# Kernel optimization log

Measured on AMD Instinct MI355X. Metric: run time of the kernel, lower is better.

The kernel has to match this reference:

```python
import jax
import jax.numpy as jnp
import numpy as np
from jax import lax

B = 4096        # batch
DATA = 16       # data_dim (control channels)
HID = 64        # hidden_dim
VFW = 128       # vf_hidden_dim
LAB = 10        # label_dim
T = 201         # number of time points in ts (span [0,1])
DT0 = 0.01      # fixed step size -> 100 Heun steps over [0,1]
N_STEPS = 100


def _linear_init(key, out_f, in_f):
    kw, kb = jax.random.split(key)
    lim = 1.0 / np.sqrt(in_f)
    w = jax.random.uniform(kw, (out_f, in_f), minval=-lim, maxval=lim, dtype=jnp.float32)
    b = jax.random.uniform(kb, (out_f,), minval=-lim, maxval=lim, dtype=jnp.float32)
    return w, b


def setup_inputs() -> dict:
    key = jax.random.key(0)
    ks = jax.random.split(key, 8)
    ts = jnp.linspace(0.0, 1.0, T, dtype=jnp.float32)
    coeffs = jax.random.normal(ks[0], (T - 1, DATA, 4), dtype=jnp.float32) * 0.1
    x0 = jax.random.normal(ks[1], (B, DATA), dtype=jnp.float32)
    lin1_w, lin1_b = _linear_init(ks[2], HID, DATA)
    mlp_w0, mlp_b0 = _linear_init(ks[3], VFW, HID)
    mlp_w1, mlp_b1 = _linear_init(ks[4], VFW, VFW)
    mlp_w2, mlp_b2 = _linear_init(ks[5], HID * DATA, VFW)
    lin2_w, lin2_b = _linear_init(ks[6], LAB, HID)
    return dict(ts=ts, coeffs=coeffs, x0=x0,
                lin1_w=lin1_w, lin1_b=lin1_b,
                mlp_w0=mlp_w0, mlp_b0=mlp_b0,
                mlp_w1=mlp_w1, mlp_b1=mlp_b1,
                mlp_w2=mlp_w2, mlp_b2=mlp_b2,
                lin2_w=lin2_w, lin2_b=lin2_b)


def reference(ts, coeffs, x0, lin1_w, lin1_b, mlp_w0, mlp_b0, mlp_w1, mlp_b1,
              mlp_w2, mlp_b2, lin2_w, lin2_b):
    def control_deriv(t):
        # cubic spline segment lookup: coeffs[idx] is (DATA, 4)
        idx = jnp.clip(jnp.searchsorted(ts[1:], t), 0, T - 2)
        dt = t - ts[idx]
        c = coeffs[idx]
        return c[:, 0] + dt * (c[:, 1] + dt * (c[:, 2] + dt * c[:, 3]))  # (DATA,)

    def vector_field(t, y):
        # MLP: HID -> VFW -> VFW -> HID*DATA (relu, relu, tanh)
        h = jax.nn.relu(y @ mlp_w0.T + mlp_b0)
        h = jax.nn.relu(h @ mlp_w1.T + mlp_b1)
        h = jnp.tanh(h @ mlp_w2.T + mlp_b2)
        vf = h.reshape(-1, HID, DATA)            # (B, HID, DATA)
        cd = control_deriv(t)                    # (DATA,)
        return jnp.einsum('bhd,d->bh', vf, cd)   # dy/dt, (B, HID)

    y0 = x0 @ lin1_w.T + lin1_b                  # (B, HID)
    t0 = ts[0]
    t1 = ts[-1]
    dt = (t1 - t0) / N_STEPS                     # == DT0 for [0,1] span

    def step(carry, _):
        y, t = carry
        k1 = vector_field(t, y)
        k2 = vector_field(t + dt, y + dt * k1)
        y_next = y + 0.5 * dt * (k1 + k2)        # Heun (explicit trapezoidal)
        return (y_next, t + dt), None

    (y_final, _), _ = lax.scan(step, (y0, t0), None, length=N_STEPS)
    logits = y_final @ lin2_w.T + lin2_b
    return jax.nn.softmax(logits, axis=-1)       # (B, LAB)
```

## Files before the change

### kernel.cpp

```cpp
#include <hip/hip_runtime.h>

#define BTOT   4096
#define DATA   16
#define HID    64
#define VFW    128
#define LAB    10
#define TPTS   201
#define NSEG   200
#define NSTEPS 100
#define MT     16
#define NBLK   (BTOT / MT)
#define YS     68

typedef __attribute__((ext_vector_type(8))) short short8;
typedef __attribute__((ext_vector_type(4))) float f32x4;

#define LOG2E  1.4426950408889634f
#define K2L    (2.0f * LOG2E)

__device__ __forceinline__ short f2bf(float f) {
    unsigned u = __builtin_bit_cast(unsigned, f);
    u = (u + 0x7FFFu + ((u >> 16) & 1u)) >> 16;
    return (short)u;
}

__device__ __forceinline__ unsigned cvt_pk_bf16(float lo, float hi) {
    unsigned r;
    asm("v_cvt_pk_bf16_f32 %0, %1, %2" : "=v"(r) : "v"(lo), "v"(hi));
    return r;
}

__device__ __forceinline__ float exp2_raw(float x) {
#if __has_builtin(__builtin_amdgcn_exp2f)
    return __builtin_amdgcn_exp2f(x);
#else
    return exp2f(x);
#endif
}

__global__ void pack_w(const float* __restrict__ W, short* __restrict__ outp,
                       int N, int K) {
    int tid = blockIdx.x * blockDim.x + threadIdx.x;
    int KS = K >> 5;
    int total = (N >> 4) * KS * 64;
    if (tid >= total) return;
    int ln = tid & 63;
    int fs = tid >> 6;
    int ks = fs % KS;
    int nt = fs / KS;
    int n  = nt * 16 + (ln & 15);
    int k0 = ks * 32 + (ln >> 4) * 8;
    const float* src = W + n * K + k0;
    short8 v;
#pragma unroll
    for (int j = 0; j < 8; ++j) v[j] = f2bf(src[j]);
    *(((short8*)outp) + tid) = v;
}

__global__ __launch_bounds__(1024, 4) void cde_main(
    const float* __restrict__ ts_g,  const float* __restrict__ coeffs,
    const float* __restrict__ x0,    const float* __restrict__ lin1_w,
    const float* __restrict__ lin1_b,
    const float* __restrict__ b0g,   const float* __restrict__ b1g,
    const float* __restrict__ b2g,   const float* __restrict__ l2w,
    const float* __restrict__ l2b,
    const short8* __restrict__ w0p,  const short8* __restrict__ w1p,
    const short8* __restrict__ w2p,  float* __restrict__ out)
{
    __shared__ float ts_sh[TPTS];
    __shared__ float ttab[NSTEPS + 1];
    __shared__ float cdtab[(NSTEPS + 1) * DATA];
    __shared__ float cdqtab[(NSTEPS + 1) * 4];
    __shared__ float y32[MT * YS];
    __shared__ __align__(16) short ybf[MT * 72];
    __shared__ __align__(16) short h1bf[MT * 136];
    __shared__ __align__(16) short h2bf[MT * 136];
    __shared__ float b2s[HID * DATA];
    __shared__ __align__(16) short w0f[1024 * 8];
    __shared__ __align__(16) short w1f[2048 * 8];
    __shared__ float lgts[MT * 12];

    const int tid  = threadIdx.x;
    const int lane = tid & 63;
    const int wave = tid >> 6;
    const int lm   = lane & 15;
    const int lg   = lane >> 4;
    const int row0 = blockIdx.x * MT;

    for (int i = tid; i < TPTS; i += 1024) ts_sh[i] = ts_g[i];
    __syncthreads();

    const float dtv = (ts_sh[TPTS - 1] - ts_sh[0]) / 100.0f;
    const float half_dt = 0.5f * dtv;

    if (tid == 0) {
        float tv = ts_sh[0];
        ttab[0] = tv;
        for (int s = 0; s < NSTEPS; ++s) { tv = tv + dtv; ttab[s + 1] = tv; }
    }
    for (int i = tid; i < HID * DATA; i += 1024) b2s[i] = b2g[i];
    for (int i = tid; i < 1024; i += 1024) ((short8*)w0f)[i] = w0p[i];
    for (int i = tid; i < 2048; i += 1024) ((short8*)w1f)[i] = w1p[i];
    for (int idx = tid; idx < MT * HID; idx += 1024) {
        int m = idx >> 6, h = idx & 63;
        float s = lin1_b[h];
        const float* xr = x0 + (row0 + m) * DATA;
        const float* wr = lin1_w + h * DATA;
#pragma unroll
        for (int k = 0; k < DATA; ++k) s += xr[k] * wr[k];
        y32[m * YS + h] = s;
        ybf[m * 72 + h] = f2bf(s);
    }
    __syncthreads();

    for (int idx = tid; idx < (NSTEPS + 1) * DATA; idx += 1024) {
        float tv = ttab[idx >> 4];
        int d = idx & 15;
        int g  = (int)(tv * 200.0f);
        int i0 = g - 2; i0 = i0 < 0 ? 0 : (i0 > 196 ? 196 : i0);
        float v0 = ts_sh[i0 + 1], v1 = ts_sh[i0 + 2], v2 = ts_sh[i0 + 3], v3 = ts_sh[i0 + 4];
        int aidx = i0 + (v0 < tv) + (v1 < tv) + (v2 < tv) + (v3 < tv);
        aidx = aidx > (NSEG - 1) ? (NSEG - 1) : aidx;
        float dtl = tv - ts_sh[aidx];
        const f32x4 cc = *(const f32x4*)(coeffs + (aidx * DATA + d) * 4);
        cdtab[idx] = cc[0] + dtl * (cc[1] + dtl * (cc[2] + dtl * cc[3]));
    }
    __syncthreads();
    for (int idx = tid; idx < (NSTEPS + 1) * 4; idx += 1024) {
        const f32x4 c = *(const f32x4*)&cdtab[idx * 4];
        cdqtab[idx] = (c[0] + c[1]) + (c[2] + c[3]);
    }

    short8 w2r[4][4];
#pragma unroll
    for (int i = 0; i < 4; ++i)
#pragma unroll
        for (int ks = 0; ks < 4; ++ks)
            w2r[i][ks] = w2p[((wave * 4 + i) * 4 + ks) * 64 + lane];
    const float bv = (wave < 8) ? b0g[wave * 16 + lm] : b1g[(wave - 8) * 16 + lm];
    __syncthreads();

    auto evalVF = [&](int tidx, float (&kv)[4]) {
        if (wave < 8) {
            short8 a0 = *(const short8*)&ybf[lm * 72 + 0  + lg * 8];
            short8 a1 = *(const short8*)&ybf[lm * 72 + 32 + lg * 8];
            short8 ws0 = ((const short8*)w0f)[(wave * 2 + 0) * 64 + lane];
            short8 ws1 = ((const short8*)w0f)[(wave * 2 + 1) * 64 + lane];
            f32x4 acc1 = {bv, bv, bv, bv};
            acc1 = __builtin_amdgcn_mfma_f32_16x16x32_bf16(a0, ws0, acc1, 0, 0, 0);
            acc1 = __builtin_amdgcn_mfma_f32_16x16x32_bf16(a1, ws1, acc1, 0, 0, 0);
            int n = wave * 16 + lm;
            unsigned p01 = cvt_pk_bf16(fmaxf(acc1[0], 0.f), fmaxf(acc1[1], 0.f));
            unsigned p23 = cvt_pk_bf16(fmaxf(acc1[2], 0.f), fmaxf(acc1[3], 0.f));
            h1bf[(4 * lg + 0) * 136 + n] = (short)p01;
            h1bf[(4 * lg + 1) * 136 + n] = (short)(p01 >> 16);
            h1bf[(4 * lg + 2) * 136 + n] = (short)p23;
            h1bf[(4 * lg + 3) * 136 + n] = (short)(p23 >> 16);
        }
        __syncthreads();
        const f32x4 cdr = *(const f32x4*)&cdtab[tidx * DATA + 4 * lg];
        const float sumcd = cdqtab[tidx * 4 + lg];
        if (wave >= 8) {
            const int nt = wave - 8;
            f32x4 acc2 = {bv, bv, bv, bv};
#pragma unroll
            for (int kp = 0; kp < 2; ++kp) {
                short8 a0 = *(const short8*)&h1bf[lm * 136 + (2 * kp) * 32 + lg * 8];
                short8 a1 = *(const short8*)&h1bf[lm * 136 + (2 * kp + 1) * 32 + lg * 8];
                short8 ws0 = ((const short8*)w1f)[(nt * 4 + 2 * kp) * 64 + lane];
                short8 ws1 = ((const short8*)w1f)[(nt * 4 + 2 * kp + 1) * 64 + lane];
                acc2 = __builtin_amdgcn_mfma_f32_16x16x32_bf16(a0, ws0, acc2, 0, 0, 0);
                acc2 = __builtin_amdgcn_mfma_f32_16x16x32_bf16(a1, ws1, acc2, 0, 0, 0);
            }
            int n = nt * 16 + lm;
            unsigned p01 = cvt_pk_bf16(fmaxf(acc2[0], 0.f), fmaxf(acc2[1], 0.f));
            unsigned p23 = cvt_pk_bf16(fmaxf(acc2[2], 0.f), fmaxf(acc2[3], 0.f));
            h2bf[(4 * lg + 0) * 136 + n] = (short)p01;
            h2bf[(4 * lg + 1) * 136 + n] = (short)(p01 >> 16);
            h2bf[(4 * lg + 2) * 136 + n] = (short)p23;
            h2bf[(4 * lg + 3) * 136 + n] = (short)(p23 >> 16);
        }
        __syncthreads();
        short8 hb[4];
#pragma unroll
        for (int ks = 0; ks < 4; ++ks)
            hb[ks] = *(const short8*)&h2bf[lm * 136 + ks * 32 + lg * 8];
#pragma unroll
        for (int i = 0; i < 4; ++i) {
            int nb = (wave * 4 + i) * 16 + 4 * lg;
            f32x4 acc = *(const f32x4*)&b2s[nb];
#pragma unroll
            for (int ks = 0; ks < 4; ++ks)
                acc = __builtin_amdgcn_mfma_f32_16x16x32_bf16(w2r[i][ks], hb[ks], acc, 0, 0, 0);
            float csum = 0.f;
#pragma unroll
            for (int r = 0; r < 4; ++r) {
                float e  = exp2_raw(acc[r] * K2L);
                float rc = __builtin_amdgcn_rcpf(e + 1.0f);
                csum = __builtin_fmaf(cdr[r], rc, csum);
            }
            float sv = __builtin_fmaf(csum, -2.0f, sumcd);
            sv += __shfl_xor(sv, 16);
            sv += __shfl_xor(sv, 32);
            kv[i] = sv;
        }
    };

    const int ycol  = wave * 4 + lg;
    const int yoff  = lm * YS + ycol;
    const int yboff = lm * 72 + ycol;
    for (int s = 0; s < NSTEPS; ++s) {
        float k1v[4], k2v[4];
        evalVF(s, k1v);
        {
            float kvv = (lg & 2) ? ((lg & 1) ? k1v[3] : k1v[2])
                                 : ((lg & 1) ? k1v[1] : k1v[0]);
            float yv = y32[yoff];
            unsigned p = cvt_pk_bf16(__builtin_fmaf(dtv, kvv, yv), 0.f);
            ybf[yboff] = (short)p;
            y32[yoff] = __builtin_fmaf(half_dt, kvv, yv);
        }
        __syncthreads();
        evalVF(s + 1, k2v);
        {
            float kvv = (lg & 2) ? ((lg & 1) ? k2v[3] : k2v[2])
                                 : ((lg & 1) ? k2v[1] : k2v[0]);
            float yn = __builtin_fmaf(half_dt, kvv, y32[yoff]);
            y32[yoff] = yn;
            unsigned p = cvt_pk_bf16(yn, 0.f);
            ybf[yboff] = (short)p;
        }
        __syncthreads();
    }

    if (tid < MT * LAB) {
        int m = tid / LAB, j = tid % LAB;
        float s = l2b[j];
        const float* wr = l2w + j * HID;
#pragma unroll
        for (int h = 0; h < HID; ++h) s += y32[m * YS + h] * wr[h];
        lgts[m * 12 + j] = s;
    }
    __syncthreads();
    if (tid < MT) {
        int m = tid;
        float mx = lgts[m * 12];
#pragma unroll
        for (int j = 1; j < LAB; ++j) mx = fmaxf(mx, lgts[m * 12 + j]);
        float e[LAB]; float sum = 0.f;
#pragma unroll
        for (int j = 0; j < LAB; ++j) { e[j] = __expf(lgts[m * 12 + j] - mx); sum += e[j]; }
#pragma unroll
        for (int j = 0; j < LAB; ++j) out[(row0 + m) * LAB + j] = e[j] / sum;
    }
}

extern "C" void kernel_launch(void* const* d_in, const int* in_sizes, int n_in,
                              void* d_out, int out_size, void* d_ws, size_t ws_size,
                              hipStream_t stream) {
    (void)in_sizes; (void)n_in; (void)out_size; (void)ws_size;
    const float* ts     = (const float*)d_in[0];
    const float* coeffs = (const float*)d_in[1];
    const float* x0     = (const float*)d_in[2];
    const float* lin1_w = (const float*)d_in[3];
    const float* lin1_b = (const float*)d_in[4];
    const float* w0     = (const float*)d_in[5];
    const float* b0     = (const float*)d_in[6];
    const float* w1     = (const float*)d_in[7];
    const float* b1     = (const float*)d_in[8];
    const float* w2     = (const float*)d_in[9];
    const float* b2     = (const float*)d_in[10];
    const float* l2w    = (const float*)d_in[11];
    const float* l2b    = (const float*)d_in[12];

    short* w0pack = (short*)d_ws;
    short* w1pack = (short*)((char*)d_ws + 16384);
    short* w2pack = (short*)((char*)d_ws + 49152);

    pack_w<<<dim3(4),  256, 0, stream>>>(w0, w0pack, 128, 64);
    pack_w<<<dim3(8),  256, 0, stream>>>(w1, w1pack, 128, 128);
    pack_w<<<dim3(64), 256, 0, stream>>>(w2, w2pack, 1024, 128);
    cde_main<<<dim3(NBLK), 1024, 0, stream>>>(ts, coeffs, x0, lin1_w, lin1_b,
        b0, b1, b2, l2w, l2b,
        (const short8*)w0pack, (const short8*)w1pack, (const short8*)w2pack,
        (float*)d_out);
}
```

Before: 412.6 us.

## Keep ODE state in registers, swap MFMA operands, vectorize hidden stores, butterfly reduce

Each lane now holds its y element in a register for the whole Heun loop instead of re-reading and re-writing fp32 y in LDS every half-step. The layer-1 and layer-2 MFMAs swap their A and B operands so the output lands transposed, which lets each lane write its four bf16 activations with one 8-byte LDS store instead of four scalar stores. The two-accumulator split shortens the MFMA dependency chain. The final cross-group reduction becomes a transpose-style butterfly using three shuffles instead of eight.

```diff
diff --git a/kernel.cpp b/kernel.cpp
--- a/kernel.cpp
+++ b/kernel.cpp
@@ -14,6 +14,7 @@
 
 typedef __attribute__((ext_vector_type(8))) short short8;
 typedef __attribute__((ext_vector_type(4))) float f32x4;
+typedef __attribute__((ext_vector_type(2))) unsigned uint2v;
 
 #define LOG2E  1.4426950408889634f
 #define K2L    (2.0f * LOG2E)
@@ -101,15 +102,17 @@
     for (int i = tid; i < HID * DATA; i += 1024) b2s[i] = b2g[i];
     for (int i = tid; i < 1024; i += 1024) ((short8*)w0f)[i] = w0p[i];
     for (int i = tid; i < 2048; i += 1024) ((short8*)w1f)[i] = w1p[i];
-    for (int idx = tid; idx < MT * HID; idx += 1024) {
-        int m = idx >> 6, h = idx & 63;
-        float s = lin1_b[h];
-        const float* xr = x0 + (row0 + m) * DATA;
-        const float* wr = lin1_w + h * DATA;
+
+    const int ycol = wave * 4 + lg;
+    float yreg;
+    {
+        float s = lin1_b[ycol];
+        const float* xr = x0 + (row0 + lm) * DATA;
+        const float* wr = lin1_w + ycol * DATA;
 #pragma unroll
         for (int k = 0; k < DATA; ++k) s += xr[k] * wr[k];
-        y32[m * YS + h] = s;
-        ybf[m * 72 + h] = f2bf(s);
+        yreg = s;
+        ybf[lm * 72 + ycol] = f2bf(s);
     }
     __syncthreads();
 
@@ -137,54 +140,55 @@
 #pragma unroll
         for (int ks = 0; ks < 4; ++ks)
             w2r[i][ks] = w2p[((wave * 4 + i) * 4 + ks) * 64 + lane];
-    const float bv = (wave < 8) ? b0g[wave * 16 + lm] : b1g[(wave - 8) * 16 + lm];
-    __syncthreads();
-
-    auto evalVF = [&](int tidx, float (&kv)[4]) {
+    const f32x4 bias4 = (wave < 8)
+        ? *(const f32x4*)&b0g[wave * 16 + 4 * lg]
+        : *(const f32x4*)&b1g[(wave - 8) * 16 + 4 * lg];
+    __syncthreads();
+
+    auto evalVF = [&](int tidx) -> float {
         if (wave < 8) {
-            short8 a0 = *(const short8*)&ybf[lm * 72 + 0  + lg * 8];
-            short8 a1 = *(const short8*)&ybf[lm * 72 + 32 + lg * 8];
+            short8 yb0 = *(const short8*)&ybf[lm * 72 + 0  + lg * 8];
+            short8 yb1 = *(const short8*)&ybf[lm * 72 + 32 + lg * 8];
             short8 ws0 = ((const short8*)w0f)[(wave * 2 + 0) * 64 + lane];
             short8 ws1 = ((const short8*)w0f)[(wave * 2 + 1) * 64 + lane];
-            f32x4 acc1 = {bv, bv, bv, bv};
-            acc1 = __builtin_amdgcn_mfma_f32_16x16x32_bf16(a0, ws0, acc1, 0, 0, 0);
-            acc1 = __builtin_amdgcn_mfma_f32_16x16x32_bf16(a1, ws1, acc1, 0, 0, 0);
-            int n = wave * 16 + lm;
-            unsigned p01 = cvt_pk_bf16(fmaxf(acc1[0], 0.f), fmaxf(acc1[1], 0.f));
-            unsigned p23 = cvt_pk_bf16(fmaxf(acc1[2], 0.f), fmaxf(acc1[3], 0.f));
-            h1bf[(4 * lg + 0) * 136 + n] = (short)p01;
-            h1bf[(4 * lg + 1) * 136 + n] = (short)(p01 >> 16);
-            h1bf[(4 * lg + 2) * 136 + n] = (short)p23;
-            h1bf[(4 * lg + 3) * 136 + n] = (short)(p23 >> 16);
+            f32x4 a = bias4;
+            f32x4 b = {0.f, 0.f, 0.f, 0.f};
+            a = __builtin_amdgcn_mfma_f32_16x16x32_bf16(ws0, yb0, a, 0, 0, 0);
+            b = __builtin_amdgcn_mfma_f32_16x16x32_bf16(ws1, yb1, b, 0, 0, 0);
+            f32x4 acc1 = a + b;
+            unsigned lo = cvt_pk_bf16(fmaxf(acc1[0], 0.f), fmaxf(acc1[1], 0.f));
+            unsigned hi = cvt_pk_bf16(fmaxf(acc1[2], 0.f), fmaxf(acc1[3], 0.f));
+            uint2v st; st[0] = lo; st[1] = hi;
+            *(uint2v*)&h1bf[lm * 136 + wave * 16 + 4 * lg] = st;
         }
         __syncthreads();
         const f32x4 cdr = *(const f32x4*)&cdtab[tidx * DATA + 4 * lg];
         const float sumcd = cdqtab[tidx * 4 + lg];
         if (wave >= 8) {
             const int nt = wave - 8;
-            f32x4 acc2 = {bv, bv, bv, bv};
-#pragma unroll
-            for (int kp = 0; kp < 2; ++kp) {
-                short8 a0 = *(const short8*)&h1bf[lm * 136 + (2 * kp) * 32 + lg * 8];
-                short8 a1 = *(const short8*)&h1bf[lm * 136 + (2 * kp + 1) * 32 + lg * 8];
-                short8 ws0 = ((const short8*)w1f)[(nt * 4 + 2 * kp) * 64 + lane];
-                short8 ws1 = ((const short8*)w1f)[(nt * 4 + 2 * kp + 1) * 64 + lane];
-                acc2 = __builtin_amdgcn_mfma_f32_16x16x32_bf16(a0, ws0, acc2, 0, 0, 0);
-                acc2 = __builtin_amdgcn_mfma_f32_16x16x32_bf16(a1, ws1, acc2, 0, 0, 0);
+            f32x4 a = bias4;
+            f32x4 b = {0.f, 0.f, 0.f, 0.f};
+#pragma unroll
+            for (int ks = 0; ks < 2; ++ks) {
+                short8 h0 = *(const short8*)&h1bf[lm * 136 + (2 * ks) * 32 + lg * 8];
+                short8 h1 = *(const short8*)&h1bf[lm * 136 + (2 * ks + 1) * 32 + lg * 8];
+                short8 ws0 = ((const short8*)w1f)[(nt * 4 + 2 * ks) * 64 + lane];
+                short8 ws1 = ((const short8*)w1f)[(nt * 4 + 2 * ks + 1) * 64 + lane];
+                a = __builtin_amdgcn_mfma_f32_16x16x32_bf16(ws0, h0, a, 0, 0, 0);
+                b = __builtin_amdgcn_mfma_f32_16x16x32_bf16(ws1, h1, b, 0, 0, 0);
             }
-            int n = nt * 16 + lm;
-            unsigned p01 = cvt_pk_bf16(fmaxf(acc2[0], 0.f), fmaxf(acc2[1], 0.f));
-            unsigned p23 = cvt_pk_bf16(fmaxf(acc2[2], 0.f), fmaxf(acc2[3], 0.f));
-            h2bf[(4 * lg + 0) * 136 + n] = (short)p01;
-            h2bf[(4 * lg + 1) * 136 + n] = (short)(p01 >> 16);
-            h2bf[(4 * lg + 2) * 136 + n] = (short)p23;
-            h2bf[(4 * lg + 3) * 136 + n] = (short)(p23 >> 16);
+            f32x4 acc2 = a + b;
+            unsigned lo = cvt_pk_bf16(fmaxf(acc2[0], 0.f), fmaxf(acc2[1], 0.f));
+            unsigned hi = cvt_pk_bf16(fmaxf(acc2[2], 0.f), fmaxf(acc2[3], 0.f));
+            uint2v st; st[0] = lo; st[1] = hi;
+            *(uint2v*)&h2bf[lm * 136 + nt * 16 + 4 * lg] = st;
         }
         __syncthreads();
         short8 hb[4];
 #pragma unroll
         for (int ks = 0; ks < 4; ++ks)
             hb[ks] = *(const short8*)&h2bf[lm * 136 + ks * 32 + lg * 8];
+        float p0, p1, p2, p3;
 #pragma unroll
         for (int i = 0; i < 4; ++i) {
             int nb = (wave * 4 + i) * 16 + 4 * lg;
@@ -200,39 +204,37 @@
                 csum = __builtin_fmaf(cdr[r], rc, csum);
             }
             float sv = __builtin_fmaf(csum, -2.0f, sumcd);
-            sv += __shfl_xor(sv, 16);
-            sv += __shfl_xor(sv, 32);
-            kv[i] = sv;
+            if (i == 0) p0 = sv; else if (i == 1) p1 = sv;
+            else if (i == 2) p2 = sv; else p3 = sv;
         }
+        bool g1 = (lg & 1) != 0;
+        float a4 = (lg & 2) ? p2 : p0;
+        float b4 = (lg & 2) ? p3 : p1;
+        float c4 = (lg & 2) ? p0 : p2;
+        float d4 = (lg & 2) ? p1 : p3;
+        float pg  = g1 ? b4 : a4;
+        float pg1 = g1 ? a4 : b4;
+        float pg2 = g1 ? d4 : c4;
+        float pg3 = g1 ? c4 : d4;
+        float s1  = pg  + __shfl_xor(pg1, 16);
+        float s1b = pg2 + __shfl_xor(pg3, 16);
+        return s1 + __shfl_xor(s1b, 32);
     };
 
-    const int ycol  = wave * 4 + lg;
-    const int yoff  = lm * YS + ycol;
     const int yboff = lm * 72 + ycol;
     for (int s = 0; s < NSTEPS; ++s) {
-        float k1v[4], k2v[4];
-        evalVF(s, k1v);
-        {
-            float kvv = (lg & 2) ? ((lg & 1) ? k1v[3] : k1v[2])
-                                 : ((lg & 1) ? k1v[1] : k1v[0]);
-            float yv = y32[yoff];
-            unsigned p = cvt_pk_bf16(__builtin_fmaf(dtv, kvv, yv), 0.f);
-            ybf[yboff] = (short)p;
-            y32[yoff] = __builtin_fmaf(half_dt, kvv, yv);
-        }
-        __syncthreads();
-        evalVF(s + 1, k2v);
-        {
-            float kvv = (lg & 2) ? ((lg & 1) ? k2v[3] : k2v[2])
-                                 : ((lg & 1) ? k2v[1] : k2v[0]);
-            float yn = __builtin_fmaf(half_dt, kvv, y32[yoff]);
-            y32[yoff] = yn;
-            unsigned p = cvt_pk_bf16(yn, 0.f);
-            ybf[yboff] = (short)p;
-        }
-        __syncthreads();
-    }
-
+        float K1 = evalVF(s);
+        ybf[yboff] = f2bf(__builtin_fmaf(dtv, K1, yreg));
+        yreg = __builtin_fmaf(half_dt, K1, yreg);
+        __syncthreads();
+        float K2 = evalVF(s + 1);
+        yreg = __builtin_fmaf(half_dt, K2, yreg);
+        ybf[yboff] = f2bf(yreg);
+        __syncthreads();
+    }
+
+    y32[lm * YS + ycol] = yreg;
+    __syncthreads();
     if (tid < MT * LAB) {
         int m = tid / LAB, j = tid % LAB;
         float s = l2b[j];
```

After: 393.2 us. 1.05x faster.
